# Kernel optimization log

Measured on AMD Instinct MI355X. Metric: run time of the kernel, lower is better.

The kernel has to match this reference:

```python
import jax, jax.numpy as jnp
import numpy as np

N, E, W, H, NXF, NDF = 131072, 8, 128, 64, 10, 4
DX = 3 + 3 * 2 * NXF  # 63
DV = 3 + 3 * 2 * NDF  # 27
TEMP = 0.166667


def pe(x, degree):
    # positional encoding: [x, sin(2^i x), cos(2^i x)]
    y = jnp.concatenate([(2.0 ** i) * x for i in range(degree)], -1)
    return jnp.concatenate([x, jnp.sin(y), jnp.cos(y)], -1)


def setup_inputs() -> dict:
    key = jax.random.key(0)
    ks = jax.random.split(key, 8)
    s = 0.05
    return {
        'x': jax.random.normal(ks[0], (N, 6), jnp.float32),
        'W_enc': jax.random.normal(ks[1], (DX, W), jnp.float32) * s,
        'b_enc': jnp.zeros((W,), jnp.float32),
        'W_sh': jax.random.normal(ks[2], (E, W, W), jnp.float32) * s,
        'b_sh': jnp.zeros((E, W), jnp.float32),
        'w_sig': jax.random.normal(ks[3], (W,), jnp.float32) * s,
        'b_sig': jnp.zeros((1,), jnp.float32),
        'W_r1': jax.random.normal(ks[4], (E, W + DV, H), jnp.float32) * s,
        'b_r1': jnp.zeros((E, H), jnp.float32),
        'W_r2': jax.random.normal(ks[5], (E, H, 3), jnp.float32) * s,
        'b_r2': jnp.zeros((E, 3), jnp.float32),
    }


def reference(x, W_enc, b_enc, W_sh, b_sh, w_sig, b_sig, W_r1, b_r1, W_r2, b_r2):
    xyz = pe(x[:, :3], NXF)          # [N, 63]
    vd = pe(x[:, 3:6], NDF)          # [N, 27]
    y = jax.nn.relu(xyz @ W_enc + b_enc)  # encoding_xyz -> [N, W]
    # all shape experts at once: [N, E, W]
    shape_out = jax.nn.relu(jnp.einsum('nd,edh->neh', y, W_sh) + b_sh)
    # shared sigma head, softplus keeps sigma > 0: [N, E]
    sigmas = jax.nn.softplus(jnp.einsum('neh,h->ne', shape_out, w_sig) + b_sig)
    log_logits = jax.nn.log_softmax(jnp.log(sigmas + 1e-10) / TEMP, axis=-1)
    # gumbel-softmax (tau=1, torch default) with fixed noise key
    u = jax.random.uniform(jax.random.key(42), sigmas.shape, jnp.float32)
    g = -jnp.log(-jnp.log(u + 1e-20) + 1e-20)
    gates_soft = jax.nn.softmax(log_logits + g, axis=-1)
    index = jnp.argmax(gates_soft, axis=-1)  # [N]
    hard = jax.nn.one_hot(index, E, dtype=sigmas.dtype)
    # straight-through hard gates
    gates_hard = hard - jax.lax.stop_gradient(gates_soft) + gates_soft
    sigmas_pooled = jnp.take_along_axis(sigmas, index[:, None], axis=-1)  # [N, 1]
    # rgb experts: concat(shape_out_i, viewdir) -> MLP -> sigmoid rgb, gated sum
    vdb = jnp.broadcast_to(vd[:, None, :], (vd.shape[0], E, DV))
    inp = jnp.concatenate([shape_out, vdb], axis=-1)  # [N, E, W+27]
    h = jax.nn.relu(jnp.einsum('nec,ech->neh', inp, W_r1) + b_r1)
    rgb = jax.nn.sigmoid(jnp.einsum('neh,eho->neo', h, W_r2) + b_r2)  # [N, E, 3]
    rgbs = jnp.sum(rgb * gates_hard[:, :, None], axis=1)  # [N, 3]
    return jnp.concatenate([rgbs, sigmas_pooled], axis=-1)  # [N, 4]
```

## Files before the change

### kernel.cpp

```cpp
#include <hip/hip_runtime.h>
#include <hip/hip_bf16.h>


#define NPTS 131072
#define PT 64
#define NTH 256
#define NBLK (NPTS / PT)
#define INV2048 (1.0f / 2048.0f)

#define WS_ENC_H 0
#define WS_ENC_L 8192
#define WS_SH_H  16384
#define WS_SH_L  147456
#define WS_R1_H  278528

#define OFF_YH   0
#define OFF_B    17408
#define OFF_VD   38912
#define OFF_RED  42496
#define OFF_GUM  51712
#define OFF_BID  53760
#define OFF_LIST 54016
#define OFF_CNT  54272
#define OFF_OFFS 54304
#define SMEM_SZ  54336

typedef __attribute__((ext_vector_type(8))) _Float16 f16x8;
typedef __attribute__((ext_vector_type(4))) float f32x4;

#define MFMA(a, b, c) __builtin_amdgcn_mfma_f32_16x16x32_f16((a), (b), (c), 0, 0, 0)

__device__ __forceinline__ unsigned rotl32(unsigned x, int d) {
  return (x << d) | (x >> (32 - d));
}

__device__ __forceinline__ float gumbel_for(unsigned flat) {
  const unsigned k0 = 0u, k1 = 42u;
  const unsigned ks2 = k0 ^ k1 ^ 0x1BD11BDAu;
  unsigned x0 = 0u + k0;
  unsigned x1 = flat + k1;
#define TF_RND(r) { x0 += x1; x1 = rotl32(x1, r); x1 ^= x0; }
  TF_RND(13) TF_RND(15) TF_RND(26) TF_RND(6)
  x0 += k1;  x1 += ks2 + 1u;
  TF_RND(17) TF_RND(29) TF_RND(16) TF_RND(24)
  x0 += ks2; x1 += k0 + 2u;
  TF_RND(13) TF_RND(15) TF_RND(26) TF_RND(6)
  x0 += k0;  x1 += k1 + 3u;
  TF_RND(17) TF_RND(29) TF_RND(16) TF_RND(24)
  x0 += k1;  x1 += ks2 + 4u;
  TF_RND(13) TF_RND(15) TF_RND(26) TF_RND(6)
  x0 += ks2; x1 += k0 + 5u;
#undef TF_RND
  unsigned bits = x0 ^ x1;
  float u = __uint_as_float((bits >> 9) | 0x3f800000u) - 1.0f;
  return -logf(-logf(u + 1e-20f) + 1e-20f);
}

__device__ __forceinline__ float dpp_rowsum16(float v) {
  int x;
  x = __builtin_amdgcn_update_dpp(0, __builtin_bit_cast(int, v), 0x128, 0xf, 0xf, true);
  v += __builtin_bit_cast(float, x);
  x = __builtin_amdgcn_update_dpp(0, __builtin_bit_cast(int, v), 0x124, 0xf, 0xf, true);
  v += __builtin_bit_cast(float, x);
  x = __builtin_amdgcn_update_dpp(0, __builtin_bit_cast(int, v), 0x122, 0xf, 0xf, true);
  v += __builtin_bit_cast(float, x);
  x = __builtin_amdgcn_update_dpp(0, __builtin_bit_cast(int, v), 0x121, 0xf, 0xf, true);
  v += __builtin_bit_cast(float, x);
  return v;
}

__global__ void prep_kernel(const float* __restrict__ W_enc,
                            const float* __restrict__ W_sh,
                            const float* __restrict__ W_r1,
                            _Float16* __restrict__ ws) {
  int idx = blockIdx.x * 256 + threadIdx.x;
  if (idx < 8192) {
    int tile = idx >> 9, r = idx & 511;
    int L = r >> 3, j = r & 7;
    int nt = tile >> 1, kt = tile & 1;
    int k = kt * 32 + (L >> 4) * 8 + j;
    int n = nt * 16 + (L & 15);
    float v = (k < 63) ? W_enc[k * 128 + n] : 0.0f;
    _Float16 h = (_Float16)v;
    ws[WS_ENC_H + idx] = h;
    ws[WS_ENC_L + idx] = (_Float16)((v - (float)h) * 2048.0f);
  } else if (idx < 8192 + 131072) {
    int s = idx - 8192;
    int tile = s >> 9, r = s & 511;
    int L = r >> 3, j = r & 7;
    int e = tile >> 5, nt = (tile >> 2) & 7, kt = tile & 3;
    int k = kt * 32 + (L >> 4) * 8 + j;
    int n = nt * 16 + (L & 15);
    float v = W_sh[e * 16384 + k * 128 + n];
    _Float16 h = (_Float16)v;
    ws[WS_SH_H + s] = h;
    ws[WS_SH_L + s] = (_Float16)((v - (float)h) * 2048.0f);
  } else if (idx < 8192 + 131072 + 81920) {
    int s = idx - (8192 + 131072);
    int tile = s >> 9, r = s & 511;
    int L = r >> 3, j = r & 7;
    int e = tile / 20, rr = tile % 20;
    int nt = rr / 5, kt = rr % 5;
    int k = kt * 32 + (L >> 4) * 8 + j;
    int n = nt * 16 + (L & 15);
    float v = (k < 155) ? W_r1[e * 9920 + k * 64 + n] : 0.0f;
    ws[WS_R1_H + s] = (_Float16)v;
  }
}

__global__ __launch_bounds__(NTH, 2)
void nerf_moe_kernel(const float* __restrict__ x,
                     const float* __restrict__ b_enc,
                     const float* __restrict__ b_sh,
                     const float* __restrict__ w_sig, const float* __restrict__ b_sig,
                     const float* __restrict__ b_r1,
                     const float* __restrict__ W_r2,  const float* __restrict__ b_r2,
                     const _Float16* __restrict__ wsw,
                     float* __restrict__ out) {
  __shared__ __align__(16) unsigned char smem[SMEM_SZ];
  _Float16* sYh  = (_Float16*)(smem + OFF_YH);
  float*    sH   = (float*)(smem + OFF_YH);
  _Float16* sYl  = (_Float16*)(smem + OFF_B);
  _Float16* sPEh = (_Float16*)(smem + OFF_B);
  _Float16* sPEl = (_Float16*)(smem + OFF_B + 9216);
  _Float16* sSB  = (_Float16*)(smem + OFF_B);
  _Float16* sVD  = (_Float16*)(smem + OFF_VD);
  float*    sRed = (float*)(smem + OFF_RED);
  float*    sGum = (float*)(smem + OFF_GUM);
  int*      sBid = (int*)(smem + OFF_BID);
  int*      sList = (int*)(smem + OFF_LIST);
  int*      sCnt = (int*)(smem + OFF_CNT);
  int*      sOff = (int*)(smem + OFF_OFFS);

  const int t  = threadIdx.x;
  const int w  = t >> 6;
  const int L  = t & 63;
  const int q  = L >> 4;
  const int c  = L & 15;
  const int n0 = blockIdx.x * PT;

  for (int idx = t; idx < PT * 64; idx += NTH) {
    int p = idx >> 6, f = idx & 63;
    const float* xr = x + (size_t)(n0 + p) * 6;
    float v;
    if (f < 3)       v = xr[f];
    else if (f < 33) { int g = f - 3;  v = sinf(xr[g % 3] * (float)(1 << (g / 3))); }
    else if (f < 63) { int g = f - 33; v = cosf(xr[g % 3] * (float)(1 << (g / 3))); }
    else             v = 0.0f;
    _Float16 h = (_Float16)v;
    sPEh[p * 72 + f] = h;
    sPEl[p * 72 + f] = (_Float16)((v - (float)h) * 2048.0f);
  }
  for (int idx = t; idx < PT * 27; idx += NTH) {
    int p = idx / 27, f = idx - p * 27;
    const float* xr = x + (size_t)(n0 + p) * 6 + 3;
    float v;
    if (f < 3)       v = xr[f];
    else if (f < 15) { int g = f - 3;  v = sinf(xr[g % 3] * (float)(1 << (g / 3))); }
    else             { int g = f - 15; v = cosf(xr[g % 3] * (float)(1 << (g / 3))); }
    sVD[p * 28 + f] = (_Float16)v;
  }
  sGum[t]       = gumbel_for((unsigned)(n0 * 8 + t));
  sGum[t + 256] = gumbel_for((unsigned)(n0 * 8 + t + 256));
  __syncthreads();

  {
    f16x8 beh[2][2], bel[2][2];
    #pragma unroll
    for (int ntL = 0; ntL < 2; ++ntL)
      #pragma unroll
      for (int kt = 0; kt < 2; ++kt) {
        int tile = (2 * w + ntL) * 2 + kt;
        beh[ntL][kt] = *(const f16x8*)(wsw + WS_ENC_H + tile * 512 + L * 8);
        bel[ntL][kt] = *(const f16x8*)(wsw + WS_ENC_L + tile * 512 + L * 8);
      }
    f16x8 pah[4][2], pal[4][2];
    #pragma unroll
    for (int mt = 0; mt < 4; ++mt)
      #pragma unroll
      for (int kt = 0; kt < 2; ++kt) {
        int off = (mt * 16 + c) * 72 + kt * 32 + q * 8;
        pah[mt][kt] = *(const f16x8*)(sPEh + off);
        pal[mt][kt] = *(const f16x8*)(sPEl + off);
      }
    f32x4 a1[4][2], a2[4][2];
    #pragma unroll
    for (int mt = 0; mt < 4; ++mt)
      #pragma unroll
      for (int ntL = 0; ntL < 2; ++ntL) { a1[mt][ntL] = (f32x4)0.0f; a2[mt][ntL] = (f32x4)0.0f; }
    #pragma unroll
    for (int kt = 0; kt < 2; ++kt)
      #pragma unroll
      for (int mt = 0; mt < 4; ++mt)
        #pragma unroll
        for (int ntL = 0; ntL < 2; ++ntL) {
          a1[mt][ntL] = MFMA(pah[mt][kt], beh[ntL][kt], a1[mt][ntL]);
          a2[mt][ntL] = MFMA(pah[mt][kt], bel[ntL][kt], a2[mt][ntL]);
          a2[mt][ntL] = MFMA(pal[mt][kt], beh[ntL][kt], a2[mt][ntL]);
        }
    __syncthreads();
    float bb0 = b_enc[(2 * w) * 16 + c];
    float bb1 = b_enc[(2 * w + 1) * 16 + c];
    #pragma unroll
    for (int mt = 0; mt < 4; ++mt)
      #pragma unroll
      for (int ntL = 0; ntL < 2; ++ntL) {
        float bb = ntL ? bb1 : bb0;
        int col = (2 * w + ntL) * 16 + c;
        #pragma unroll
        for (int r = 0; r < 4; ++r) {
          float v = fmaxf(a1[mt][ntL][r] + a2[mt][ntL][r] * INV2048 + bb, 0.0f);
          int row = mt * 16 + q * 4 + r;
          _Float16 h = (_Float16)v;
          sYh[row * 136 + col] = h;
          sYl[row * 136 + col] = (_Float16)((v - (float)h) * 2048.0f);
        }
      }
  }
  __syncthreads();

  f16x8 Ah[4][4], Al[4][4];
  #pragma unroll
  for (int mt = 0; mt < 4; ++mt)
    #pragma unroll
    for (int kt = 0; kt < 4; ++kt) {
      int off = (mt * 16 + c) * 136 + kt * 32 + q * 8;
      Ah[mt][kt] = *(const f16x8*)(sYh + off);
      Al[mt][kt] = *(const f16x8*)(sYl + off);
    }
  const float ws0 = w_sig[(2 * w) * 16 + c];
  const float ws1 = w_sig[(2 * w + 1) * 16 + c];
  const bool b3 = (c & 8) != 0, b2g = (c & 4) != 0, b1 = (c & 2) != 0, b0 = (c & 1) != 0;

  float sigAcc[8];
  #pragma unroll 1
  for (int e = 0; e < 8; ++e) {
    float sp[16];
    #pragma unroll
    for (int i = 0; i < 16; ++i) sp[i] = 0.0f;
    #pragma unroll
    for (int ntL = 0; ntL < 2; ++ntL) {
      f32x4 a1[4], a2[4];
      #pragma unroll
      for (int mt = 0; mt < 4; ++mt) { a1[mt] = (f32x4)0.0f; a2[mt] = (f32x4)0.0f; }
      #pragma unroll
      for (int kt = 0; kt < 4; ++kt) {
        int tile = (e * 8 + 2 * w + ntL) * 4 + kt;
        f16x8 bh = *(const f16x8*)(wsw + WS_SH_H + tile * 512 + L * 8);
        f16x8 bl = *(const f16x8*)(wsw + WS_SH_L + tile * 512 + L * 8);
        #pragma unroll
        for (int mt = 0; mt < 4; ++mt) {
          a1[mt] = MFMA(Ah[mt][kt], bh, a1[mt]);
          a2[mt] = MFMA(Ah[mt][kt], bl, a2[mt]);
          a2[mt] = MFMA(Al[mt][kt], bh, a2[mt]);
        }
      }
      float wsC = ntL ? ws1 : ws0;
      float bb = b_sh[e * 128 + (2 * w + ntL) * 16 + c];
      #pragma unroll
      for (int mt = 0; mt < 4; ++mt)
        #pragma unroll
        for (int r = 0; r < 4; ++r) {
          float s = fmaxf(a1[mt][r] + a2[mt][r] * INV2048 + bb, 0.0f);
          sp[mt * 4 + r] = fmaf(s, wsC, sp[mt * 4 + r]);
        }
    }
    #pragma unroll
    for (int i = 0; i < 16; ++i) sp[i] = dpp_rowsum16(sp[i]);
    float u0 = b2g ? sp[4]  : sp[0],  u1 = b2g ? sp[5]  : sp[1];
    float u2 = b2g ? sp[6]  : sp[2],  u3 = b2g ? sp[7]  : sp[3];
    float v0 = b2g ? sp[12] : sp[8],  v1 = b2g ? sp[13] : sp[9];
    float v2 = b2g ? sp[14] : sp[10], v3 = b2g ? sp[15] : sp[11];
    float r0 = b3 ? v0 : u0, r1 = b3 ? v1 : u1, r2 = b3 ? v2 : u2, r3 = b3 ? v3 : u3;
    float rr = b1 ? (b0 ? r3 : r2) : (b0 ? r1 : r0);
    sigAcc[e] = rr;
  }
  {
    int R = (c >> 2) * 16 + q * 4 + (c & 3);
    f32x4 g0 = { sigAcc[0], sigAcc[1], sigAcc[2], sigAcc[3] };
    f32x4 g1 = { sigAcc[4], sigAcc[5], sigAcc[6], sigAcc[7] };
    *(f32x4*)(sRed + R * 36 + w * 8)     = g0;
    *(f32x4*)(sRed + R * 36 + w * 8 + 4) = g1;
  }
  __syncthreads();

  if (t < PT) {
    float best = 0.0f, bsig = 0.0f;
    int bide = 0;
    const float bs = b_sig[0];
    #pragma unroll
    for (int e = 0; e < 8; ++e) {
      float s = sRed[t * 36 + e] + sRed[t * 36 + 8 + e] +
                sRed[t * 36 + 16 + e] + sRed[t * 36 + 24 + e];
      float dotv = s + bs;
      float sig = fmaxf(dotv, 0.0f) + log1pf(expf(-fabsf(dotv)));
      float z = logf(sig + 1e-10f) / 0.166667f;
      float score = z + sGum[t * 8 + e];
      if (e == 0 || score > best) { best = score; bsig = sig; bide = e; }
    }
    sBid[t] = bide;
    out[(size_t)(n0 + t) * 4 + 3] = bsig;
  }
  __syncthreads();

  if (t < 8) {
    int cnt = 0;
    for (int p = 0; p < PT; ++p) cnt += (sBid[p] == t);
    sCnt[t] = cnt;
  }
  __syncthreads();
  if (t < 8) {
    int off = 0;
    for (int i = 0; i < t; ++i) off += sCnt[i];
    sOff[t] = off;
    int k = off;
    for (int p = 0; p < PT; ++p) if (sBid[p] == t) sList[k++] = p;
  }
  __syncthreads();

  for (int idx = t; idx < PT * 32; idx += NTH) {
    int s = idx >> 5, cc = idx & 31;
    _Float16 v = (cc < 27) ? sVD[sList[s] * 28 + cc] : (_Float16)0.0f;
    sSB[s * 168 + 128 + cc] = v;
  }
  #pragma unroll 1
  for (int ei = 0; ei < 2; ++ei) {
    int e = 2 * w + ei;
    int cnt = sCnt[e], off = sOff[e];
    for (int base = 0; base < cnt; base += 16) {
      int sidx = base + c; if (sidx >= cnt) sidx = cnt - 1;
      int pt = sList[off + sidx];
      f16x8 ah[4];
      #pragma unroll
      for (int kt = 0; kt < 4; ++kt)
        ah[kt] = *(const f16x8*)(sYh + pt * 136 + kt * 32 + q * 8);
      f32x4 acc[8];
      #pragma unroll
      for (int nt = 0; nt < 8; ++nt) acc[nt] = (f32x4)0.0f;
      #pragma unroll
      for (int nt = 0; nt < 8; ++nt)
        #pragma unroll
        for (int kt = 0; kt < 4; ++kt) {
          f16x8 b = *(const f16x8*)(wsw + WS_SH_H + ((e * 8 + nt) * 4 + kt) * 512 + L * 8);
          acc[nt] = MFMA(ah[kt], b, acc[nt]);
        }
      #pragma unroll
      for (int nt = 0; nt < 8; ++nt) {
        float bb = b_sh[e * 128 + nt * 16 + c];
        #pragma unroll
        for (int r = 0; r < 4; ++r) {
          int m = q * 4 + r;
          if (base + m < cnt)
            sSB[(off + base + m) * 168 + nt * 16 + c] =
                (_Float16)fmaxf(acc[nt][r] + bb, 0.0f);
        }
      }
    }
  }
  __syncthreads();

  #pragma unroll 1
  for (int ei = 0; ei < 2; ++ei) {
    int e = 2 * w + ei;
    int cnt = sCnt[e], off = sOff[e];
    for (int base = 0; base < cnt; base += 16) {
      int sidx = base + c; if (sidx >= cnt) sidx = cnt - 1;
      int slot = off + sidx;
      f16x8 ag[5];
      #pragma unroll
      for (int kt = 0; kt < 5; ++kt)
        ag[kt] = *(const f16x8*)(sSB + slot * 168 + kt * 32 + q * 8);
      f32x4 hacc[4];
      #pragma unroll
      for (int nt = 0; nt < 4; ++nt) hacc[nt] = (f32x4)0.0f;
      #pragma unroll
      for (int nt = 0; nt < 4; ++nt)
        #pragma unroll
        for (int kt = 0; kt < 5; ++kt) {
          f16x8 bf = *(const f16x8*)(wsw + WS_R1_H + ((e * 4 + nt) * 5 + kt) * 512 + L * 8);
          hacc[nt] = MFMA(ag[kt], bf, hacc[nt]);
        }
      #pragma unroll
      for (int nt = 0; nt < 4; ++nt) {
        float bb = b_r1[e * 64 + nt * 16 + c];
        #pragma unroll
        for (int r = 0; r < 4; ++r) {
          int m = q * 4 + r;
          if (base + m < cnt)
            sH[(off + base + m) * 68 + nt * 16 + c] = fmaxf(hacc[nt][r] + bb, 0.0f);
        }
      }
    }
  }
  __syncthreads();

  if (t < 192) {
    int s = t / 3, o = t - s * 3;
    int pt = sList[s];
    int e = sBid[pt];
    float a = b_r2[e * 3 + o];
    const float* w2 = W_r2 + e * 192 + o;
    #pragma unroll 8
    for (int j = 0; j < 64; ++j)
      a = fmaf(sH[s * 68 + j], w2[j * 3], a);
    out[(size_t)(n0 + pt) * 4 + o] = 1.0f / (1.0f + expf(-a));
  }
}

extern "C" void kernel_launch(void* const* d_in, const int* in_sizes, int n_in,
                              void* d_out, int out_size, void* d_ws, size_t ws_size,
                              hipStream_t stream) {
  (void)in_sizes; (void)n_in; (void)ws_size; (void)out_size;
  const float* x     = (const float*)d_in[0];
  const float* W_enc = (const float*)d_in[1];
  const float* b_enc = (const float*)d_in[2];
  const float* W_sh  = (const float*)d_in[3];
  const float* b_sh  = (const float*)d_in[4];
  const float* w_sig = (const float*)d_in[5];
  const float* b_sig = (const float*)d_in[6];
  const float* W_r1  = (const float*)d_in[7];
  const float* b_r1  = (const float*)d_in[8];
  const float* W_r2  = (const float*)d_in[9];
  const float* b_r2  = (const float*)d_in[10];
  _Float16* ws = (_Float16*)d_ws;
  float* outp = (float*)d_out;
  prep_kernel<<<864, 256, 0, stream>>>(W_enc, W_sh, W_r1, ws);
  nerf_moe_kernel<<<NBLK, NTH, 0, stream>>>(x, b_enc, b_sh, w_sig, b_sig,
                                            b_r1, W_r2, b_r2, ws, outp);
}
```

Before: 287.0 us.

## Swap MFMA operand order, drop sVD buffer, raise occupancy to 3 blocks

The sigma expert GEMM swaps its MFMA operands so weights become the A operand. Per-point sums then reduce within a thread and go through a small shared buffer each expert, which replaces the DPP row sums and the 16-float selection logic. The low-half Y fragments are reloaded from LDS on each use instead of held in registers. View-direction positional encodings are computed only in the gather step, which removes the sVD buffer and shrinks shared memory. Together with launch_bounds raised to 3 blocks per CU, the aim is higher occupancy, at the cost of two extra block barriers per expert and repeated LDS reads.

Result: slower. 522.0 us (+81.9%).

```diff
diff --git a/kernel.cpp b/kernel.cpp
--- a/kernel.cpp
+++ b/kernel.cpp
@@ -16,16 +16,16 @@
 
 #define OFF_YH   0
 #define OFF_B    17408
-#define OFF_VD   38912
-#define OFF_RED  42496
-#define OFF_GUM  51712
-#define OFF_BID  53760
-#define OFF_LIST 54016
-#define OFF_CNT  54272
-#define OFF_OFFS 54304
-#define SMEM_SZ  54336
+#define OFF_RED  38912
+#define OFF_GUM  44032
+#define OFF_BID  46080
+#define OFF_LIST 46336
+#define OFF_CNT  46592
+#define OFF_OFFS 46624
+#define SMEM_SZ  46656
 
 typedef __attribute__((ext_vector_type(8))) _Float16 f16x8;
+typedef __attribute__((ext_vector_type(4))) _Float16 f16x4;
 typedef __attribute__((ext_vector_type(4))) float f32x4;
 
 #define MFMA(a, b, c) __builtin_amdgcn_mfma_f32_16x16x32_f16((a), (b), (c), 0, 0, 0)
@@ -54,19 +54,6 @@
   unsigned bits = x0 ^ x1;
   float u = __uint_as_float((bits >> 9) | 0x3f800000u) - 1.0f;
   return -logf(-logf(u + 1e-20f) + 1e-20f);
-}
-
-__device__ __forceinline__ float dpp_rowsum16(float v) {
-  int x;
-  x = __builtin_amdgcn_update_dpp(0, __builtin_bit_cast(int, v), 0x128, 0xf, 0xf, true);
-  v += __builtin_bit_cast(float, x);
-  x = __builtin_amdgcn_update_dpp(0, __builtin_bit_cast(int, v), 0x124, 0xf, 0xf, true);
-  v += __builtin_bit_cast(float, x);
-  x = __builtin_amdgcn_update_dpp(0, __builtin_bit_cast(int, v), 0x122, 0xf, 0xf, true);
-  v += __builtin_bit_cast(float, x);
-  x = __builtin_amdgcn_update_dpp(0, __builtin_bit_cast(int, v), 0x121, 0xf, 0xf, true);
-  v += __builtin_bit_cast(float, x);
-  return v;
 }
 
 __global__ void prep_kernel(const float* __restrict__ W_enc,
@@ -108,7 +95,7 @@
   }
 }
 
-__global__ __launch_bounds__(NTH, 2)
+__global__ __launch_bounds__(NTH, 3)
 void nerf_moe_kernel(const float* __restrict__ x,
                      const float* __restrict__ b_enc,
                      const float* __restrict__ b_sh,
@@ -124,13 +111,13 @@
   _Float16* sPEh = (_Float16*)(smem + OFF_B);
   _Float16* sPEl = (_Float16*)(smem + OFF_B + 9216);
   _Float16* sSB  = (_Float16*)(smem + OFF_B);
-  _Float16* sVD  = (_Float16*)(smem + OFF_VD);
   float*    sRed = (float*)(smem + OFF_RED);
   float*    sGum = (float*)(smem + OFF_GUM);
   int*      sBid = (int*)(smem + OFF_BID);
   int*      sList = (int*)(smem + OFF_LIST);
   int*      sCnt = (int*)(smem + OFF_CNT);
   int*      sOff = (int*)(smem + OFF_OFFS);
+  float*    sBsc = sGum + 448;
 
   const int t  = threadIdx.x;
   const int w  = t >> 6;
@@ -138,6 +125,7 @@
   const int q  = L >> 4;
   const int c  = L & 15;
   const int n0 = blockIdx.x * PT;
+  (void)sBsc;
 
   for (int idx = t; idx < PT * 64; idx += NTH) {
     int p = idx >> 6, f = idx & 63;
@@ -151,15 +139,6 @@
     sPEh[p * 72 + f] = h;
     sPEl[p * 72 + f] = (_Float16)((v - (float)h) * 2048.0f);
   }
-  for (int idx = t; idx < PT * 27; idx += NTH) {
-    int p = idx / 27, f = idx - p * 27;
-    const float* xr = x + (size_t)(n0 + p) * 6 + 3;
-    float v;
-    if (f < 3)       v = xr[f];
-    else if (f < 15) { int g = f - 3;  v = sinf(xr[g % 3] * (float)(1 << (g / 3))); }
-    else             { int g = f - 15; v = cosf(xr[g % 3] * (float)(1 << (g / 3))); }
-    sVD[p * 28 + f] = (_Float16)v;
-  }
   sGum[t]       = gumbel_for((unsigned)(n0 * 8 + t));
   sGum[t + 256] = gumbel_for((unsigned)(n0 * 8 + t + 256));
   __syncthreads();
@@ -219,85 +198,68 @@
   }
   __syncthreads();
 
-  f16x8 Ah[4][4], Al[4][4];
+  f16x8 Ah[4][4];
   #pragma unroll
-  for (int mt = 0; mt < 4; ++mt)
-    #pragma unroll
-    for (int kt = 0; kt < 4; ++kt) {
-      int off = (mt * 16 + c) * 136 + kt * 32 + q * 8;
-      Ah[mt][kt] = *(const f16x8*)(sYh + off);
-      Al[mt][kt] = *(const f16x8*)(sYl + off);
-    }
-  const float ws0 = w_sig[(2 * w) * 16 + c];
-  const float ws1 = w_sig[(2 * w + 1) * 16 + c];
-  const bool b3 = (c & 8) != 0, b2g = (c & 4) != 0, b1 = (c & 2) != 0, b0 = (c & 1) != 0;
-
-  float sigAcc[8];
+  for (int nt = 0; nt < 4; ++nt)
+    #pragma unroll
+    for (int kt = 0; kt < 4; ++kt)
+      Ah[nt][kt] = *(const f16x8*)(sYh + (nt * 16 + c) * 136 + kt * 32 + q * 8);
+  const f32x4 wsv0 = *(const f32x4*)(w_sig + (2 * w) * 16 + q * 4);
+  const f32x4 wsv1 = *(const f32x4*)(w_sig + (2 * w + 1) * 16 + q * 4);
+  const float bs = b_sig[0];
+
+  float best = 0.0f, bsig = 0.0f;
+  int bide = 0;
+
   #pragma unroll 1
   for (int e = 0; e < 8; ++e) {
-    float sp[16];
-    #pragma unroll
-    for (int i = 0; i < 16; ++i) sp[i] = 0.0f;
-    #pragma unroll
-    for (int ntL = 0; ntL < 2; ++ntL) {
+    float psum[4] = {0.f, 0.f, 0.f, 0.f};
+    #pragma unroll
+    for (int i = 0; i < 2; ++i) {
       f32x4 a1[4], a2[4];
       #pragma unroll
-      for (int mt = 0; mt < 4; ++mt) { a1[mt] = (f32x4)0.0f; a2[mt] = (f32x4)0.0f; }
+      for (int nt = 0; nt < 4; ++nt) { a1[nt] = (f32x4)0.0f; a2[nt] = (f32x4)0.0f; }
       #pragma unroll
       for (int kt = 0; kt < 4; ++kt) {
-        int tile = (e * 8 + 2 * w + ntL) * 4 + kt;
+        int tile = (e * 8 + 2 * w + i) * 4 + kt;
         f16x8 bh = *(const f16x8*)(wsw + WS_SH_H + tile * 512 + L * 8);
         f16x8 bl = *(const f16x8*)(wsw + WS_SH_L + tile * 512 + L * 8);
         #pragma unroll
-        for (int mt = 0; mt < 4; ++mt) {
-          a1[mt] = MFMA(Ah[mt][kt], bh, a1[mt]);
-          a2[mt] = MFMA(Ah[mt][kt], bl, a2[mt]);
-          a2[mt] = MFMA(Al[mt][kt], bh, a2[mt]);
-        }
-      }
-      float wsC = ntL ? ws1 : ws0;
-      float bb = b_sh[e * 128 + (2 * w + ntL) * 16 + c];
-      #pragma unroll
-      for (int mt = 0; mt < 4; ++mt)
+        for (int nt = 0; nt < 4; ++nt) {
+          f16x8 al = *(const f16x8*)(sYl + (nt * 16 + c) * 136 + kt * 32 + q * 8);
+          a1[nt] = MFMA(bh, Ah[nt][kt], a1[nt]);
+          a2[nt] = MFMA(bl, Ah[nt][kt], a2[nt]);
+          a2[nt] = MFMA(bh, al, a2[nt]);
+        }
+      }
+      f32x4 bb = *(const f32x4*)(b_sh + e * 128 + (2 * w + i) * 16 + q * 4);
+      f32x4 wv = i ? wsv1 : wsv0;
+      #pragma unroll
+      for (int nt = 0; nt < 4; ++nt)
         #pragma unroll
         for (int r = 0; r < 4; ++r) {
-          float s = fmaxf(a1[mt][r] + a2[mt][r] * INV2048 + bb, 0.0f);
-          sp[mt * 4 + r] = fmaf(s, wsC, sp[mt * 4 + r]);
+          float s = fmaxf(fmaf(a2[nt][r], INV2048, a1[nt][r]) + bb[r], 0.0f);
+          psum[nt] = fmaf(s, wv[r], psum[nt]);
         }
     }
     #pragma unroll
-    for (int i = 0; i < 16; ++i) sp[i] = dpp_rowsum16(sp[i]);
-    float u0 = b2g ? sp[4]  : sp[0],  u1 = b2g ? sp[5]  : sp[1];
-    float u2 = b2g ? sp[6]  : sp[2],  u3 = b2g ? sp[7]  : sp[3];
-    float v0 = b2g ? sp[12] : sp[8],  v1 = b2g ? sp[13] : sp[9];
-    float v2 = b2g ? sp[14] : sp[10], v3 = b2g ? sp[15] : sp[11];
-    float r0 = b3 ? v0 : u0, r1 = b3 ? v1 : u1, r2 = b3 ? v2 : u2, r3 = b3 ? v3 : u3;
-    float rr = b1 ? (b0 ? r3 : r2) : (b0 ? r1 : r0);
-    sigAcc[e] = rr;
-  }
-  {
-    int R = (c >> 2) * 16 + q * 4 + (c & 3);
-    f32x4 g0 = { sigAcc[0], sigAcc[1], sigAcc[2], sigAcc[3] };
-    f32x4 g1 = { sigAcc[4], sigAcc[5], sigAcc[6], sigAcc[7] };
-    *(f32x4*)(sRed + R * 36 + w * 8)     = g0;
-    *(f32x4*)(sRed + R * 36 + w * 8 + 4) = g1;
-  }
-  __syncthreads();
-
-  if (t < PT) {
-    float best = 0.0f, bsig = 0.0f;
-    int bide = 0;
-    const float bs = b_sig[0];
-    #pragma unroll
-    for (int e = 0; e < 8; ++e) {
-      float s = sRed[t * 36 + e] + sRed[t * 36 + 8 + e] +
-                sRed[t * 36 + 16 + e] + sRed[t * 36 + 24 + e];
+    for (int nt = 0; nt < 4; ++nt)
+      sRed[(nt * 16 + c) * 20 + w * 4 + q] = psum[nt];
+    __syncthreads();
+    if (t < PT) {
+      const f32x4* rp = (const f32x4*)(sRed + t * 20);
+      f32x4 p0 = rp[0], p1 = rp[1], p2 = rp[2], p3 = rp[3];
+      float s = ((p0.x + p0.y) + (p0.z + p0.w)) + ((p1.x + p1.y) + (p1.z + p1.w)) +
+                ((p2.x + p2.y) + (p2.z + p2.w)) + ((p3.x + p3.y) + (p3.z + p3.w));
       float dotv = s + bs;
       float sig = fmaxf(dotv, 0.0f) + log1pf(expf(-fabsf(dotv)));
       float z = logf(sig + 1e-10f) / 0.166667f;
       float score = z + sGum[t * 8 + e];
       if (e == 0 || score > best) { best = score; bsig = sig; bide = e; }
     }
+    __syncthreads();
+  }
+  if (t < PT) {
     sBid[t] = bide;
     out[(size_t)(n0 + t) * 4 + 3] = bsig;
   }
@@ -320,8 +282,14 @@
 
   for (int idx = t; idx < PT * 32; idx += NTH) {
     int s = idx >> 5, cc = idx & 31;
-    _Float16 v = (cc < 27) ? sVD[sList[s] * 28 + cc] : (_Float16)0.0f;
-    sSB[s * 168 + 128 + cc] = v;
+    int pt = sList[s];
+    const float* xr = x + (size_t)(n0 + pt) * 6 + 3;
+    float v;
+    if (cc < 3)       v = xr[cc];
+    else if (cc < 15) { int g = cc - 3;  v = sinf(xr[g % 3] * (float)(1 << (g / 3))); }
+    else if (cc < 27) { int g = cc - 15; v = cosf(xr[g % 3] * (float)(1 << (g / 3))); }
+    else              v = 0.0f;
+    sSB[s * 168 + 128 + cc] = (_Float16)v;
   }
   #pragma unroll 1
   for (int ei = 0; ei < 2; ++ei) {
@@ -330,30 +298,30 @@
     for (int base = 0; base < cnt; base += 16) {
       int sidx = base + c; if (sidx >= cnt) sidx = cnt - 1;
       int pt = sList[off + sidx];
-      f16x8 ah[4];
+      f16x8 yb[4];
       #pragma unroll
       for (int kt = 0; kt < 4; ++kt)
-        ah[kt] = *(const f16x8*)(sYh + pt * 136 + kt * 32 + q * 8);
+        yb[kt] = *(const f16x8*)(sYh + pt * 136 + kt * 32 + q * 8);
       f32x4 acc[8];
       #pragma unroll
-      for (int nt = 0; nt < 8; ++nt) acc[nt] = (f32x4)0.0f;
-      #pragma unroll
-      for (int nt = 0; nt < 8; ++nt)
+      for (int jt = 0; jt < 8; ++jt) acc[jt] = (f32x4)0.0f;
+      #pragma unroll
+      for (int jt = 0; jt < 8; ++jt)
         #pragma unroll
         for (int kt = 0; kt < 4; ++kt) {
-          f16x8 b = *(const f16x8*)(wsw + WS_SH_H + ((e * 8 + nt) * 4 + kt) * 512 + L * 8);
-          acc[nt] = MFMA(ah[kt], b, acc[nt]);
-        }
-      #pragma unroll
-      for (int nt = 0; nt < 8; ++nt) {
-        float bb = b_sh[e * 128 + nt * 16 + c];
-        #pragma unroll
-        for (int r = 0; r < 4; ++r) {
-          int m = q * 4 + r;
-          if (base + m < cnt)
-            sSB[(off + base + m) * 168 + nt * 16 + c] =
-                (_Float16)fmaxf(acc[nt][r] + bb, 0.0f);
-        }
+          f16x8 a = *(const f16x8*)(wsw + WS_SH_H + ((e * 8 + jt) * 4 + kt) * 512 + L * 8);
+          acc[jt] = MFMA(a, yb[kt], acc[jt]);
+        }
+      bool wr = (base + c) < cnt;
+      int slot = off + base + c;
+      #pragma unroll
+      for (int jt = 0; jt < 8; ++jt) {
+        f32x4 bb = *(const f32x4*)(b_sh + e * 128 + jt * 16 + q * 4);
+        f16x4 v;
+        #pragma unroll
+        for (int r = 0; r < 4; ++r)
+          v[r] = (_Float16)fmaxf(acc[jt][r] + bb[r], 0.0f);
+        if (wr) *(f16x4*)(sSB + slot * 168 + jt * 16 + q * 4) = v;
       }
     }
   }
@@ -400,9 +368,14 @@
     int e = sBid[pt];
     float a = b_r2[e * 3 + o];
     const float* w2 = W_r2 + e * 192 + o;
-    #pragma unroll 8
-    for (int j = 0; j < 64; ++j)
-      a = fmaf(sH[s * 68 + j], w2[j * 3], a);
+    #pragma unroll
+    for (int jj = 0; jj < 64; jj += 4) {
+      f32x4 h4 = *(const f32x4*)(sH + s * 68 + jj);
+      a = fmaf(h4.x, w2[jj * 3], a);
+      a = fmaf(h4.y, w2[jj * 3 + 3], a);
+      a = fmaf(h4.z, w2[jj * 3 + 6], a);
+      a = fmaf(h4.w, w2[jj * 3 + 9], a);
+    }
     out[(size_t)(n0 + pt) * 4 + o] = 1.0f / (1.0f + expf(-a));
   }
 }
```
